# Kernel optimization log

Measured on AMD Instinct MI355X. Metric: run time of the kernel, lower is better.

Reference implementation:

```python
import jax, jax.numpy as jnp
import numpy as np

B, C, D = 4096, 100, 384
EPS = 1e-12


def setup_inputs() -> dict:
    key = jax.random.key(0)
    k1, k2, k3, k4 = jax.random.split(key, 4)
    return {
        "inputs": jax.random.normal(k1, (B, D), dtype=jnp.float32),
        "centers": jax.random.normal(k2, (C, D), dtype=jnp.float32),          # nn.Parameter torch.randn
        "centers_weights": jax.random.uniform(k3, (C, D), dtype=jnp.float32),  # nn.Parameter torch.rand
        "targets": jax.random.randint(k4, (B,), 0, C, dtype=jnp.int64),
        "epoch_number": 10,
    }


def _weighted_sqdist(x, y, w):
    # dist2[i, j] = sum_d w[j, d] * (y[j, d] - x[i, d])**2, computed via GEMMs
    a = jnp.sum(w * y * y, axis=1)            # [J]
    cross = x @ (w * y).T                     # [I, J]
    quad = (x * x) @ w.T                      # [I, J]
    return a[None, :] - 2.0 * cross + quad


def reference(inputs, centers, centers_weights, targets, epoch_number):
    bsz = inputs.shape[0]
    w2 = 2.0 ** centers_weights                                        # [C, D]

    # calc_centers(which_one=1): distance of each center to its nearest other center.
    # Original goes through numpy -> detached from autograd, hence stop_gradient.
    cd2 = _weighted_sqdist(centers, centers, w2).T                     # cd2[i,j] uses w2[i]
    cd = jnp.sqrt(jnp.maximum(cd2, 0.0))                               # [C, C]
    centers_dist = jax.lax.stop_gradient(jnp.sort(cd, axis=1)[:, 1])   # [C]

    cb = centers[targets]                                              # [B, D] gathered centers
    wb = w2[targets]                                                   # [B, D] gathered 2**weights
    # dist[i, j] = sqrt(sum_d wb[j,d] * (cb[j,d] - inputs[i,d])**2)
    dist2 = _weighted_sqdist(inputs, cb, wb)                           # [B, B]
    dist = jnp.sqrt(jnp.clip(dist2, EPS))

    mask = targets[:, None] == targets[None, :]                        # same-class mask
    dist_ap = jnp.max(jnp.where(mask, dist, -jnp.inf), axis=1)         # hardest positive
    dist_an = jnp.min(jnp.where(mask, jnp.inf, dist), axis=1)          # hardest negative

    cc = centers_dist[targets]                                         # [B]
    loss_i = jnp.where(dist_an >= cc, dist_ap, dist_ap - dist_an + cc)
    return jnp.sum(loss_i) / bsz
```

## Files before the change

kernel.cpp:

```cpp
#include <hip/hip_runtime.h>
#include <math.h>

#define B_N 4096
#define C_N 100
#define CPAD 112
#define D_N 384
#define EPSF 1e-12f
#define NTILES 7
#define NKT24 24
#define NRT 64
#define NAB 288
#define GRID_MAIN 504

typedef __attribute__((ext_vector_type(8))) short short8;
typedef __attribute__((ext_vector_type(4))) float f32x4;

static __device__ __forceinline__ short f2bf(float f) {
    unsigned u = __float_as_uint(f);
    u = (u + 0x7FFFu + ((u >> 16) & 1u)) >> 16;
    return (short)u;
}


__global__ __launch_bounds__(256) void k_prep(const float* __restrict__ inputs,
                                              const float* __restrict__ centers,
                                              const float* __restrict__ cw,
                                              const int* __restrict__ targets,
                                              ushort* __restrict__ bfrag,
                                              ushort* __restrict__ afrag,
                                              float* __restrict__ a2,
                                              int* __restrict__ present,
                                              int* __restrict__ apmax,
                                              int* __restrict__ anmin,
                                              int* __restrict__ cdminI) {
    int bid = blockIdx.x, t = threadIdx.x;

    if (bid < CPAD) {
        int c = bid;
        int nt = c >> 4, col = c & 15;
        __shared__ float sred[4];
        __shared__ int ps[4];

        float acc = 0.f;
        if (c < C_N) {
            for (int d = t; d < D_N; d += 256) {
                float wv = exp2f(cw[c * D_N + d]);
                float ce = centers[c * D_N + d];
                float p  = wv * ce;
                acc = fmaf(p, ce, acc);
                int kt = d >> 5, kr = d & 31, lg = kr >> 3, e = kr & 7;
                bfrag[(((nt * 24 + kt)      * 4 + lg) * 16 + col) * 8 + e] =
                    (ushort)f2bf(wv);
                bfrag[(((nt * 24 + kt + 12) * 4 + lg) * 16 + col) * 8 + e] =
                    (ushort)f2bf(-2.f * p);
            }
        } else {
            for (int d = t; d < D_N; d += 256) {
                int kt = d >> 5, kr = d & 31, lg = kr >> 3, e = kr & 7;
                bfrag[(((nt * 24 + kt)      * 4 + lg) * 16 + col) * 8 + e] = 0;
                bfrag[(((nt * 24 + kt + 12) * 4 + lg) * 16 + col) * 8 + e] = 0;
            }
        }
        for (int m = 1; m < 64; m <<= 1) acc += __shfl_xor(acc, m, 64);

        int pr = 0;
        if (c < C_N)
            for (int i = t; i < B_N; i += 256) pr |= (targets[i] == c) ? 1 : 0;
        pr = __any(pr) ? 1 : 0;

        if ((t & 63) == 0) { sred[t >> 6] = acc; ps[t >> 6] = pr; }

        int idx = bid * 256 + t;
        if (idx < B_N) {
            apmax[idx] = 0;
            anmin[idx] = 0x7F800000;
        }
        if (bid == 0 && t < CPAD) cdminI[t] = 0x7F800000;

        __syncthreads();
        if (t == 0) {
            a2[c] = (c < C_N) ? ((sred[0] + sred[1]) + (sred[2] + sred[3])) : 0.f;
            present[c] = (c < C_N) ? (ps[0] | ps[1] | ps[2] | ps[3]) : 0;
        }
    } else {
        int j = bid - CPAD;
        int s = j & 7;
        int i = j >> 3;
        int rt = s + 8 * (i >> 2);
        int w  = i & 3;
        if (rt >= NRT + 2) return;
        int g = (rt < NRT) ? (rt * 4 + w) : (256 + (rt - NRT) * 4 + w);

#pragma unroll
        for (int it = 0; it < 3; it++) {
            int cid = t + it * 256;
            int row = cid & 15;
            int kc  = cid >> 4;
            const float* src;
            if (g < 256) {
                src = inputs + (size_t)(g * 16 + row) * D_N;
            } else {
                int cr = min((g - 256) * 16 + row, C_N - 1);
                src = centers + (size_t)cr * D_N;
            }
            float4 v0 = *(const float4*)(src + kc * 8);
            float4 v1 = *(const float4*)(src + kc * 8 + 4);
            short8 ox, ox2;
            ox[0] = f2bf(v0.x); ox[1] = f2bf(v0.y);
            ox[2] = f2bf(v0.z); ox[3] = f2bf(v0.w);
            ox[4] = f2bf(v1.x); ox[5] = f2bf(v1.y);
            ox[6] = f2bf(v1.z); ox[7] = f2bf(v1.w);
            ox2[0] = f2bf(v0.x * v0.x); ox2[1] = f2bf(v0.y * v0.y);
            ox2[2] = f2bf(v0.z * v0.z); ox2[3] = f2bf(v0.w * v0.w);
            ox2[4] = f2bf(v1.x * v1.x); ox2[5] = f2bf(v1.y * v1.y);
            ox2[6] = f2bf(v1.z * v1.z); ox2[7] = f2bf(v1.w * v1.w);
            int kt = kc >> 2, lg = kc & 3;
            *(short8*)(afrag + (size_t)(((g * 24 + kt)      * 4 + lg) * 16 + row) * 8) = ox2;
            *(short8*)(afrag + (size_t)(((g * 24 + kt + 12) * 4 + lg) * 16 + row) * 8) = ox;
        }
    }
}

__global__ __launch_bounds__(256) void k_main(const ushort* __restrict__ afrag,
                                              const ushort* __restrict__ bfrag,
                                              const int* __restrict__ targets,
                                              const float* __restrict__ a2g,
                                              const int* __restrict__ present,
                                              int* __restrict__ apmax,
                                              int* __restrict__ anmin,
                                              int* __restrict__ cdminI) {
    int b = blockIdx.x;
    int xs  = b & 7;
    int q   = b >> 3;
    int nt  = q % 7;
    int rtg = q / 7;
    int rt  = xs + 8 * rtg;
    if (rt >= NRT + 2) return;

    int tid = threadIdx.x;
    int w   = tid >> 6;
    int l   = tid & 63;
    int c0  = nt * 16;
    bool isc = (rt >= NRT);

    int g = isc ? (256 + (rt - NRT) * 4 + w) : (rt * 4 + w);
    int slot = (l >> 4) * 16 + (l & 15);

    const short8* A = (const short8*)afrag + (size_t)g * 24 * 64;
    const short8* B = (const short8*)bfrag + (size_t)nt * 24 * 64;

    f32x4 acc0 = {0.f, 0.f, 0.f, 0.f};
    f32x4 acc1 = {0.f, 0.f, 0.f, 0.f};
#pragma unroll 8
    for (int kt = 0; kt < NKT24; kt++) {
        short8 a = A[kt * 64 + slot];
        short8 bb = B[kt * 64 + slot];
        if (kt & 1) acc1 = __builtin_amdgcn_mfma_f32_16x16x32_bf16(a, bb, acc1, 0, 0, 0);
        else        acc0 = __builtin_amdgcn_mfma_f32_16x16x32_bf16(a, bb, acc0, 0, 0, 0);
    }
    f32x4 acc = acc0 + acc1;

    int c = c0 + (l & 15);
    float a2v = a2g[c];
    int prs = present[c];

    if (!isc) {
#pragma unroll
        for (int r = 0; r < 4; r++) {
            float gv = sqrtf(fmaxf(a2v + acc[r], EPSF));
            int rw  = w * 16 + (l >> 4) * 4 + r;
            int row = rt * 64 + rw;
            int ti  = targets[row];
            float ap = (c == ti) ? gv : -1.f;
            float an = (prs && c != ti) ? gv : INFINITY;
#pragma unroll
            for (int m = 1; m < 16; m <<= 1) {
                ap = fmaxf(ap, __shfl_xor(ap, m, 64));
                an = fminf(an, __shfl_xor(an, m, 64));
            }
            if ((l & 15) == 0) {
                if (ap > 0.f) atomicMax(&apmax[row], __float_as_int(ap));
                atomicMin(&anmin[row], __float_as_int(an));
            }
        }
    } else {
        float m = INFINITY;
#pragma unroll
        for (int r = 0; r < 4; r++) {
            float gv = sqrtf(fmaxf(a2v + acc[r], EPSF));
            int jg = (rt - NRT) * 64 + w * 16 + (l >> 4) * 4 + r;
            if (jg < C_N && jg != c) m = fminf(m, gv);
        }
        m = fminf(m, __shfl_xor(m, 16, 64));
        m = fminf(m, __shfl_xor(m, 32, 64));
        if (l < 16 && c < C_N && m < INFINITY)
            atomicMin(&cdminI[c], __float_as_int(m));
    }
}

__global__ __launch_bounds__(1024) void k_final(const int* __restrict__ apmax,
                                                const int* __restrict__ anmin,
                                                const int* __restrict__ cdminI,
                                                const int* __restrict__ targets,
                                                float* __restrict__ out) {
    int tid = threadIdx.x;
    __shared__ float cd_s[C_N];
    if (tid < C_N) cd_s[tid] = __int_as_float(cdminI[tid]);
    __syncthreads();

    float sum = 0.f;
    for (int row = tid; row < B_N; row += 1024) {
        float ap = __int_as_float(apmax[row]);
        float an = __int_as_float(anmin[row]);
        float cc = cd_s[targets[row]];
        sum += (an >= cc) ? ap : (ap - an + cc);
    }
    for (int m = 1; m < 64; m <<= 1) sum += __shfl_xor(sum, m, 64);
    __shared__ float sw[16];
    if ((tid & 63) == 0) sw[tid >> 6] = sum;
    __syncthreads();
    if (tid < 64) {
        float v = (tid < 16) ? sw[tid] : 0.f;
        for (int m = 1; m < 16; m <<= 1) v += __shfl_xor(v, m, 64);
        if (tid == 0) out[0] = v / (float)B_N;
    }
}

extern "C" void kernel_launch(void* const* d_in, const int* in_sizes, int n_in,
                              void* d_out, int out_size, void* d_ws, size_t ws_size,
                              hipStream_t stream) {
    const float* inputs  = (const float*)d_in[0];
    const float* centers = (const float*)d_in[1];
    const float* cw      = (const float*)d_in[2];
    const int*   targets = (const int*)d_in[3];
    (void)in_sizes; (void)n_in; (void)out_size; (void)ws_size;

    char* ws = (char*)d_ws;
    ushort* bfrag   = (ushort*)(ws + 0);
    ushort* afrag   = (ushort*)(ws + 172032);
    int*    apmax   = (int*)  (ws + 6660096);
    int*    anmin   = (int*)  (ws + 6676480);
    float*  a2      = (float*)(ws + 6692864);
    int*    present = (int*)  (ws + 6693376);
    int*    cdminI  = (int*)  (ws + 6693888);

    k_prep<<<CPAD + NAB, 256, 0, stream>>>(inputs, centers, cw, targets,
                                           bfrag, afrag, a2, present,
                                           apmax, anmin, cdminI);
    k_main<<<GRID_MAIN, 256, 0, stream>>>(afrag, bfrag, targets, a2, present,
                                          apmax, anmin, cdminI);
    k_final<<<1, 1024, 0, stream>>>(apmax, anmin, cdminI, targets, (float*)d_out);
}
```

Measured before the change: 19.34 us.

## Split K across the four waves and reduce partial MFMA sums through LDS

Each block now handles a single 16-row group instead of four, and its four waves each compute a quarter of the K dimension (6 of 24 k-tiles). The partial accumulators are then summed through shared memory by wave 0, which runs the epilogue. The grid is four times larger. The aim is more parallelism and shorter per-wave dependency chains, at the cost of an LDS reduction, a barrier and three idle waves during the epilogue.

```diff
diff --git a/kernel.cpp b/kernel.cpp
--- a/kernel.cpp
+++ b/kernel.cpp
@@ -10,7 +10,7 @@
 #define NKT24 24
 #define NRT 64
 #define NAB 288
-#define GRID_MAIN 504
+#define GRID_MAIN 2016
 
 typedef __attribute__((ext_vector_type(8))) short short8;
 typedef __attribute__((ext_vector_type(4))) float f32x4;
@@ -129,12 +129,15 @@
                                               int* __restrict__ apmax,
                                               int* __restrict__ anmin,
                                               int* __restrict__ cdminI) {
+    __shared__ __align__(16) f32x4 red[3][64];
+
     int b = blockIdx.x;
-    int xs  = b & 7;
-    int q   = b >> 3;
-    int nt  = q % 7;
-    int rtg = q / 7;
-    int rt  = xs + 8 * rtg;
+    int xs = b & 7;
+    int q  = b >> 3;
+    int nt = q % 7;
+    int i  = q / 7;
+    int rt = xs + 8 * (i >> 2);
+    int gs = i & 3;
     if (rt >= NRT + 2) return;
 
     int tid = threadIdx.x;
@@ -143,22 +146,24 @@
     int c0  = nt * 16;
     bool isc = (rt >= NRT);
 
-    int g = isc ? (256 + (rt - NRT) * 4 + w) : (rt * 4 + w);
+    int g = isc ? (256 + (rt - NRT) * 4 + gs) : (rt * 4 + gs);
     int slot = (l >> 4) * 16 + (l & 15);
 
-    const short8* A = (const short8*)afrag + (size_t)g * 24 * 64;
-    const short8* B = (const short8*)bfrag + (size_t)nt * 24 * 64;
-
-    f32x4 acc0 = {0.f, 0.f, 0.f, 0.f};
-    f32x4 acc1 = {0.f, 0.f, 0.f, 0.f};
-#pragma unroll 8
-    for (int kt = 0; kt < NKT24; kt++) {
+    const short8* A = (const short8*)afrag + (size_t)g * 24 * 64 + w * 6 * 64;
+    const short8* B = (const short8*)bfrag + (size_t)nt * 24 * 64 + w * 6 * 64;
+
+    f32x4 acc = {0.f, 0.f, 0.f, 0.f};
+#pragma unroll
+    for (int kt = 0; kt < 6; kt++) {
         short8 a = A[kt * 64 + slot];
         short8 bb = B[kt * 64 + slot];
-        if (kt & 1) acc1 = __builtin_amdgcn_mfma_f32_16x16x32_bf16(a, bb, acc1, 0, 0, 0);
-        else        acc0 = __builtin_amdgcn_mfma_f32_16x16x32_bf16(a, bb, acc0, 0, 0, 0);
-    }
-    f32x4 acc = acc0 + acc1;
+        acc = __builtin_amdgcn_mfma_f32_16x16x32_bf16(a, bb, acc, 0, 0, 0);
+    }
+
+    if (w > 0) red[w - 1][l] = acc;
+    __syncthreads();
+    if (w > 0) return;
+    acc = ((acc + red[0][l]) + (red[1][l] + red[2][l]));
 
     int c = c0 + (l & 15);
     float a2v = a2g[c];
@@ -168,8 +173,7 @@
 #pragma unroll
         for (int r = 0; r < 4; r++) {
             float gv = sqrtf(fmaxf(a2v + acc[r], EPSF));
-            int rw  = w * 16 + (l >> 4) * 4 + r;
-            int row = rt * 64 + rw;
+            int row = g * 16 + (l >> 4) * 4 + r;
             int ti  = targets[row];
             float ap = (c == ti) ? gv : -1.f;
             float an = (prs && c != ti) ? gv : INFINITY;
@@ -188,7 +192,7 @@
 #pragma unroll
         for (int r = 0; r < 4; r++) {
             float gv = sqrtf(fmaxf(a2v + acc[r], EPSF));
-            int jg = (rt - NRT) * 64 + w * 16 + (l >> 4) * 4 + r;
+            int jg = (g - 256) * 16 + (l >> 4) * 4 + r;
             if (jg < C_N && jg != c) m = fminf(m, gv);
         }
         m = fminf(m, __shfl_xor(m, 16, 64));
```

Result: slower. 20.30 us (median of 2 runs) (+4.9%).
